# Optimization experiments

Hardware: AMD Instinct MI355X
Metric: run time of the kernel (lower is better)

## Reference

```python
import jax, jax.numpy as jnp
import numpy as np

D_MODEL = 1024
N_HEADS = 16
HEAD_DIM = 64
T = 4096
ROT = HEAD_DIM // 2          # 32 channels get rotary
PAIR = ROT // 2              # 16 cos/sin frequencies
EPS = 1e-6
SCALE = 0.12                 # constant attention scale (not 1/sqrt(d))
ROPE_BASE = 10000.0
VOCAB = 50257


def setup_inputs() -> dict:
    key = jax.random.key(0)
    k_x, k_qkv, k_o, k_tok = jax.random.split(key, 4)
    bound = 0.5 / np.sqrt(D_MODEL)
    x = jax.random.normal(k_x, (1, T, D_MODEL), dtype=jnp.float32)
    w_qkv = jax.random.uniform(k_qkv, (3 * D_MODEL, D_MODEL), jnp.float32, -bound, bound)
    # module uses zero_init for w_o; use small random so output is non-trivial
    w_o = jax.random.uniform(k_o, (D_MODEL, D_MODEL), jnp.float32, -bound, bound)
    q_norm_w = jnp.ones((HEAD_DIM,), jnp.float32)
    k_norm_w = jnp.ones((HEAD_DIM,), jnp.float32)
    tokens = jax.random.randint(k_tok, (1, T), 0, VOCAB, dtype=jnp.int64)
    pos = jnp.arange(T, dtype=jnp.int64)
    # RotaryCache: inv_freq over pair dims, cos/sin of t * inv_freq
    inv_freq = 1.0 / (ROPE_BASE ** (jnp.arange(PAIR, dtype=jnp.float32) / PAIR))
    freqs = jnp.arange(T, dtype=jnp.float32)[:, None] * inv_freq[None, :]  # [T, PAIR]
    return {
        "x": x, "tokens": tokens, "pos": pos,
        "w_qkv": w_qkv, "w_o": w_o,
        "q_norm_w": q_norm_w, "k_norm_w": k_norm_w,
        "cos": jnp.cos(freqs), "sin": jnp.sin(freqs),
        "window_tokens": 1024, "block_size": 128,
    }


def _rmsnorm(x, w):
    var = jnp.mean(x * x, axis=-1, keepdims=True)
    return x * jax.lax.rsqrt(var + EPS) * w


def reference(x, tokens, pos, w_qkv, w_o, q_norm_w, k_norm_w, cos, sin,
              window_tokens, block_size):
    B, Tq, C = x.shape
    H, Dh = N_HEADS, HEAD_DIM
    qkv = x @ w_qkv.T                                  # [B, T, 3C]
    q, k, v = jnp.split(qkv, 3, axis=-1)

    def to_bhtd(t):
        return t.reshape(B, Tq, H, Dh).transpose(0, 2, 1, 3)
    q, k, v = to_bhtd(q), to_bhtd(k), to_bhtd(v)

    q = _rmsnorm(q, q_norm_w)
    k = _rmsnorm(k, k_norm_w)

    # half-truncated RoPE: rotate first ROT channels pairwise (even/odd)
    c = cos[pos][None, None]                           # [1,1,T,PAIR]
    s = sin[pos][None, None]

    def rope_rotate(t):
        t1, t2 = t[..., :ROT], t[..., ROT:]
        even, odd = t1[..., 0::2], t1[..., 1::2]
        r_even = even * c - odd * s
        r_odd = even * s + odd * c
        t1r = jnp.stack([r_even, r_odd], axis=-1).reshape(t1.shape)
        return jnp.concatenate([t1r, t2], axis=-1)

    q = rope_rotate(q)
    k = rope_rotate(k)

    v = v * 0.5                                        # no value-embed branch

    scores = jnp.einsum('bhtd,bhsd->bhts', q, k) * SCALE
    idx = jnp.arange(Tq)
    diff = idx[:, None] - idx[None, :]
    allowed = (diff >= 0) & (diff < window_tokens)     # sliding causal window
    scores = jnp.where(allowed, scores, -jnp.inf)
    p = jax.nn.softmax(scores, axis=-1)
    out = jnp.einsum('bhts,bhsd->bhtd', p, v)
    out = out.transpose(0, 2, 1, 3).reshape(B, Tq, C)
    return out @ w_o.T
```

## Files before the change

### kernel.cpp

```cpp
#include <hip/hip_runtime.h>


typedef __bf16 bf16x8 __attribute__((ext_vector_type(8)));
typedef __bf16 bf16x2 __attribute__((ext_vector_type(2)));
typedef float f32x4 __attribute__((ext_vector_type(4)));
typedef unsigned short u16x8 __attribute__((ext_vector_type(8)));
typedef unsigned short u16x4 __attribute__((ext_vector_type(4)));

#define MFMA16(a, b, c) __builtin_amdgcn_mfma_f32_16x16x32_bf16((a), (b), (c), 0, 0, 0)

__device__ __forceinline__ unsigned short f2bf(float f) {
    unsigned int u = __float_as_uint(f);
    u += 0x7fffu + ((u >> 16) & 1u);
    return (unsigned short)(u >> 16);
}
__device__ __forceinline__ float bf2f(unsigned short h) {
    return __uint_as_float(((unsigned int)h) << 16);
}
__device__ __forceinline__ unsigned int pk2bf(float a, float b) {
#if __has_builtin(__builtin_amdgcn_cvt_pk_bf16_f32)
    bf16x2 v = __builtin_amdgcn_cvt_pk_bf16_f32(a, b);
    return __builtin_bit_cast(unsigned int, v);
#else
    return (unsigned int)f2bf(a) | ((unsigned int)f2bf(b) << 16);
#endif
}

__device__ __forceinline__ void gl_lds16(const void* g, void* l) {
    typedef __attribute__((address_space(1))) unsigned int GU;
    typedef __attribute__((address_space(3))) unsigned int LU;
    __builtin_amdgcn_global_load_lds((GU*)(unsigned long long)g,
                                     (LU*)(unsigned int)(unsigned long long)l,
                                     16, 0, 0);
}

__global__ void cvt3_kernel(const float* __restrict__ x,
                            const float* __restrict__ wqkv,
                            const float* __restrict__ wo,
                            unsigned short* __restrict__ xb,
                            unsigned short* __restrict__ wqkvb,
                            unsigned short* __restrict__ wob) {
    int i = blockIdx.x * 256 + threadIdx.x;
    const float* src;
    unsigned short* dst;
    int off;
    if (i < 1048576) { src = x; dst = xb; off = i; }
    else if (i < 1835008) { src = wqkv; dst = wqkvb; off = i - 1048576; }
    else { src = wo; dst = wob; off = i - 1835008; }
    float4 f = ((const float4*)src)[off];
    u16x4 o;
    o[0] = f2bf(f.x); o[1] = f2bf(f.y); o[2] = f2bf(f.z); o[3] = f2bf(f.w);
    ((u16x4*)dst)[off] = o;
}

#define TBS 72
__global__ __launch_bounds__(256) void gemm_qkv(
    const unsigned short* __restrict__ A,
    const unsigned short* __restrict__ Bt,
    const float* __restrict__ cosb, const float* __restrict__ sinb,
    const float* __restrict__ qw, const float* __restrict__ kw,
    unsigned short* __restrict__ Qb,
    unsigned short* __restrict__ Kb,
    unsigned short* __restrict__ Vt)
{
    __shared__ unsigned short As[2][128 * 32];
    __shared__ unsigned short Bs[2][128 * 32];
    __shared__ unsigned short tb[4][16 * TBS];
    const int tid = threadIdx.x;
    const int wave = tid >> 6, lane = tid & 63;
    const int quad = lane >> 4, l16 = lane & 15;
    const int m0 = blockIdx.x * 128, n0 = blockIdx.y * 128;
    const int wm = (wave >> 1) * 64;

    f32x4 acc[4][4];
#pragma unroll
    for (int i = 0; i < 4; ++i)
#pragma unroll
        for (int j = 0; j < 4; ++j) acc[i][j] = (f32x4){0.f, 0.f, 0.f, 0.f};

    auto stageAB = [&](int buf, int k0) {
#pragma unroll
        for (int i = 0; i < 2; ++i) {
            const int c = wave * 2 + i;
            const int e = (c * 64 + lane) * 8;
            const int r = e >> 5, col = e & 31;
            gl_lds16(A + (size_t)(m0 + r) * 1024 + (k0 + col), &As[buf][c * 512]);
            gl_lds16(Bt + (size_t)(n0 + r) * 1024 + (k0 + col), &Bs[buf][c * 512]);
        }
    };

    stageAB(0, 0);
    __syncthreads();
    int buf = 0;
    for (int k0 = 0; k0 < 1024; k0 += 32) {
        if (k0 + 32 < 1024) stageAB(buf ^ 1, k0 + 32);
        bf16x8 af[4], bfr[4];
#pragma unroll
        for (int mt = 0; mt < 4; ++mt)
            af[mt] = *(const bf16x8*)&As[buf][(wm + mt * 16 + l16) * 32 + quad * 8];
#pragma unroll
        for (int nt = 0; nt < 4; ++nt)
            bfr[nt] = *(const bf16x8*)&Bs[buf][((wave & 1) * 64 + nt * 16 + l16) * 32 + quad * 8];
#pragma unroll
        for (int mt = 0; mt < 4; ++mt)
#pragma unroll
            for (int nt = 0; nt < 4; ++nt)
                acc[mt][nt] = MFMA16(af[mt], bfr[nt], acc[mt][nt]);
        __syncthreads();
        buf ^= 1;
    }

    const int region = blockIdx.y >> 3;
    const int h = ((blockIdx.y & 7) << 1) + (wave & 1);
    unsigned short* tbw = tb[wave];

    if (region < 2) {
        const float* wgt = region ? kw : qw;
        unsigned short* dst = region ? Kb : Qb;
        float w[4];
#pragma unroll
        for (int nt = 0; nt < 4; ++nt) w[nt] = wgt[nt * 16 + l16];
#pragma unroll
        for (int mt = 0; mt < 4; ++mt) {
#pragma unroll
            for (int r = 0; r < 4; ++r) {
                const int row = m0 + wm + mt * 16 + quad * 4 + r;
                float ss = 0.f;
#pragma unroll
                for (int nt = 0; nt < 4; ++nt)
                    ss += acc[mt][nt][r] * acc[mt][nt][r];
                ss += __shfl_xor(ss, 1); ss += __shfl_xor(ss, 2);
                ss += __shfl_xor(ss, 4); ss += __shfl_xor(ss, 8);
                const float rn = rsqrtf(ss * (1.f / 64.f) + 1e-6f);
                float val[4];
#pragma unroll
                for (int nt = 0; nt < 4; ++nt)
                    val[nt] = acc[mt][nt][r] * rn * w[nt];
#pragma unroll
                for (int nt = 0; nt < 2; ++nt) {
                    const float prt = __shfl_xor(val[nt], 1);
                    const int p = nt * 8 + (l16 >> 1);
                    const float c = cosb[row * 16 + p];
                    const float s = sinb[row * 16 + p];
                    val[nt] = (l16 & 1) ? (prt * s + val[nt] * c)
                                        : (val[nt] * c - prt * s);
                }
#pragma unroll
                for (int nt = 0; nt < 4; ++nt)
                    tbw[(quad * 4 + r) * TBS + nt * 16 + l16] = f2bf(val[nt]);
            }
            const int t = lane >> 2, dcol = (lane & 3) * 16;
            u16x8 v0 = *(const u16x8*)&tbw[t * TBS + dcol];
            u16x8 v1 = *(const u16x8*)&tbw[t * TBS + dcol + 8];
            const size_t ob = ((size_t)h * 4096 + (m0 + wm + mt * 16 + t)) * 64 + dcol;
            *(u16x8*)&dst[ob] = v0;
            *(u16x8*)&dst[ob + 8] = v1;
        }
    } else {
#pragma unroll
        for (int mt = 0; mt < 4; ++mt) {
#pragma unroll
            for (int nt = 0; nt < 4; ++nt)
#pragma unroll
                for (int r = 0; r < 4; ++r)
                    tbw[(nt * 16 + l16) * 16 + quad * 4 + r] =
                        f2bf(acc[mt][nt][r] * 0.5f);
            u16x8 v0 = *(const u16x8*)&tbw[lane * 16];
            u16x8 v1 = *(const u16x8*)&tbw[lane * 16 + 8];
            const size_t vo = ((size_t)h * 64 + lane) * 4096 + m0 + wm + mt * 16;
            *(u16x8*)&Vt[vo] = v0;
            *(u16x8*)&Vt[vo + 8] = v1;
        }
    }
}

#define PSTR 72

template <int MODE>
__device__ __forceinline__ void attn_compute(
    int s0, int tq, int quad, int l16,
    const unsigned short* Ks0, const unsigned short* Ks1,
    const unsigned short* Vs0, const unsigned short* Vs1,
    unsigned short* Pw,
    const bf16x8 qf0, const bf16x8 qf1, f32x4 (&o)[4], float& lsum)
{
    const float c = 0.17312340490667046f;
#pragma unroll
    for (int i = 0; i < 4; ++i) {
        const bf16x8 kf0 = *(const bf16x8*)&Ks0[(i * 16 + l16) * 32 + quad * 8];
        const bf16x8 kf1 = *(const bf16x8*)&Ks1[(i * 16 + l16) * 32 + quad * 8];
        f32x4 z = (f32x4){0.f, 0.f, 0.f, 0.f};
        z = MFMA16(kf0, qf0, z);
        z = MFMA16(kf1, qf1, z);
        float p[4];
#pragma unroll
        for (int r = 0; r < 4; ++r) {
            float e = exp2f(z[r] * c);
            if (MODE == 1) {
                const int s = s0 + i * 16 + quad * 4 + r;
                e = ((tq - s) < 1024) ? e : 0.f;
            }
            if (MODE == 2) {
                const int s = s0 + i * 16 + quad * 4 + r;
                e = (s <= tq) ? e : 0.f;
            }
            p[r] = e;
            lsum += e;
        }
        uint2 pk;
        pk.x = pk2bf(p[0], p[1]);
        pk.y = pk2bf(p[2], p[3]);
        *(uint2*)&Pw[l16 * PSTR + i * 16 + quad * 4] = pk;
    }
    const bf16x8 pf0 = *(const bf16x8*)&Pw[l16 * PSTR + quad * 8];
    const bf16x8 pf1 = *(const bf16x8*)&Pw[l16 * PSTR + 32 + quad * 8];
#pragma unroll
    for (int dt = 0; dt < 4; ++dt) {
        const bf16x8 vf0 = *(const bf16x8*)&Vs0[(dt * 16 + l16) * 32 + quad * 8];
        const bf16x8 vf1 = *(const bf16x8*)&Vs1[(dt * 16 + l16) * 32 + quad * 8];
        o[dt] = MFMA16(pf0, vf0, o[dt]);
        o[dt] = MFMA16(pf1, vf1, o[dt]);
    }
}

__global__ __launch_bounds__(256) void attn_kernel(
    const unsigned short* __restrict__ Qb,
    const unsigned short* __restrict__ Kb,
    const unsigned short* __restrict__ Vt,
    unsigned short* __restrict__ att)
{
    __shared__ unsigned short Ks0[2][64 * 32];
    __shared__ unsigned short Ks1[2][64 * 32];
    __shared__ unsigned short Vs0[2][64 * 32];
    __shared__ unsigned short Vs1[2][64 * 32];
    __shared__ unsigned short P[4][16 * PSTR];

    const int bid = blockIdx.x;
    const int h = ((bid & 7) << 1) | ((bid >> 3) & 1);
    const int t0 = (bid >> 4) * 64;

    const int tid = threadIdx.x;
    const int wave = tid >> 6, lane = tid & 63;
    const int quad = lane >> 4, l16 = lane & 15;
    const int qt0 = t0 + wave * 16;
    const int tq = qt0 + l16;
    const int krow = tid >> 2, kcol = (tid & 3) * 8;

    const unsigned short* Qh = Qb + (size_t)h * 4096 * 64;
    const unsigned short* Kh = Kb + (size_t)h * 4096 * 64;
    const unsigned short* Vh = Vt + (size_t)h * 64 * 4096;

    const bf16x8 qf0 = *(const bf16x8*)&Qh[(qt0 + l16) * 64 + quad * 8];
    const bf16x8 qf1 = *(const bf16x8*)&Qh[(qt0 + l16) * 64 + 32 + quad * 8];

    f32x4 o[4];
#pragma unroll
    for (int dt = 0; dt < 4; ++dt) o[dt] = (f32x4){0.f, 0.f, 0.f, 0.f};
    float lsum = 0.f;
    unsigned short* Pw = P[wave];

    auto stage = [&](int buf, int s0) {
        const unsigned short* kb = Kh + (size_t)(s0 + krow) * 64 + kcol;
        const unsigned short* vb = Vh + (size_t)krow * 4096 + s0 + kcol;
        gl_lds16(kb,      &Ks0[buf][wave * 512]);
        gl_lds16(kb + 32, &Ks1[buf][wave * 512]);
        gl_lds16(vb,      &Vs0[buf][wave * 512]);
        gl_lds16(vb + 32, &Vs1[buf][wave * 512]);
    };

    const int sbase = (t0 >= 1024) ? (t0 - 1024) : 0;
    stage(0, sbase);
    __syncthreads();
    int buf = 0;
    for (int s0 = sbase; s0 <= t0; s0 += 64) {
        if (s0 + 64 <= t0) stage(buf ^ 1, s0 + 64);
        if (s0 == sbase && t0 >= 1024)
            attn_compute<1>(s0, tq, quad, l16, Ks0[buf], Ks1[buf], Vs0[buf],
                            Vs1[buf], Pw, qf0, qf1, o, lsum);
        else if (s0 == t0)
            attn_compute<2>(s0, tq, quad, l16, Ks0[buf], Ks1[buf], Vs0[buf],
                            Vs1[buf], Pw, qf0, qf1, o, lsum);
        else
            attn_compute<0>(s0, tq, quad, l16, Ks0[buf], Ks1[buf], Vs0[buf],
                            Vs1[buf], Pw, qf0, qf1, o, lsum);
        __syncthreads();
        buf ^= 1;
    }

    lsum += __shfl_xor(lsum, 16);
    lsum += __shfl_xor(lsum, 32);
    float lr[4];
#pragma unroll
    for (int r = 0; r < 4; ++r) lr[r] = 1.f / __shfl(lsum, quad * 4 + r);
#pragma unroll
    for (int dt = 0; dt < 4; ++dt)
#pragma unroll
        for (int r = 0; r < 4; ++r)
            att[(size_t)(qt0 + quad * 4 + r) * 1024 + h * 64 + dt * 16 + l16] =
                f2bf(o[dt][r] * lr[r]);
}

template <int BM, bool F32OUT>
__global__ __launch_bounds__(256) void gemm_bt(
    const unsigned short* __restrict__ A,
    const unsigned short* __restrict__ Bt,
    void* __restrict__ Cp, int N, int K) {
    __shared__ unsigned short As[2][BM * 32];
    __shared__ unsigned short Bs[2][128 * 32];
    constexpr int MT = BM / 32;
    const int tid = threadIdx.x;
    const int wave = tid >> 6, lane = tid & 63;
    const int quad = lane >> 4, l16 = lane & 15;
    const int m0 = blockIdx.x * BM, n0 = blockIdx.y * 128;
    const int wm = (wave >> 1) * (BM / 2), wn = (wave & 1) * 64;

    f32x4 acc[MT][4];
#pragma unroll
    for (int i = 0; i < MT; ++i)
#pragma unroll
        for (int j = 0; j < 4; ++j) acc[i][j] = (f32x4){0.f, 0.f, 0.f, 0.f};

    auto stageAB = [&](int buf, int k0) {
#pragma unroll
        for (int i = 0; i < BM / 64; ++i) {
            const int c = wave * (BM / 64) + i;
            const int e = (c * 64 + lane) * 8;
            const int r = e >> 5, col = e & 31;
            gl_lds16(A + (size_t)(m0 + r) * K + (k0 + col), &As[buf][c * 512]);
        }
#pragma unroll
        for (int i = 0; i < 2; ++i) {
            const int c = wave * 2 + i;
            const int e = (c * 64 + lane) * 8;
            const int r = e >> 5, col = e & 31;
            gl_lds16(Bt + (size_t)(n0 + r) * K + (k0 + col), &Bs[buf][c * 512]);
        }
    };

    stageAB(0, 0);
    __syncthreads();
    int buf = 0;
    for (int k0 = 0; k0 < K; k0 += 32) {
        if (k0 + 32 < K) stageAB(buf ^ 1, k0 + 32);
        bf16x8 af[MT], bfr[4];
#pragma unroll
        for (int mt = 0; mt < MT; ++mt)
            af[mt] = *(const bf16x8*)&As[buf][(wm + mt * 16 + l16) * 32 + quad * 8];
#pragma unroll
        for (int nt = 0; nt < 4; ++nt)
            bfr[nt] = *(const bf16x8*)&Bs[buf][(wn + nt * 16 + l16) * 32 + quad * 8];
#pragma unroll
        for (int mt = 0; mt < MT; ++mt)
#pragma unroll
            for (int nt = 0; nt < 4; ++nt)
                acc[mt][nt] = MFMA16(af[mt], bfr[nt], acc[mt][nt]);
        __syncthreads();
        buf ^= 1;
    }
#pragma unroll
    for (int mt = 0; mt < MT; ++mt)
#pragma unroll
        for (int nt = 0; nt < 4; ++nt)
#pragma unroll
            for (int r = 0; r < 4; ++r) {
                const int row = m0 + wm + mt * 16 + quad * 4 + r;
                const int col = n0 + wn + nt * 16 + l16;
                const float v = acc[mt][nt][r];
                if (F32OUT)
                    ((float*)Cp)[(size_t)row * N + col] = v;
                else
                    ((unsigned short*)Cp)[(size_t)row * N + col] = f2bf(v);
            }
}

extern "C" void kernel_launch(void* const* d_in, const int* in_sizes, int n_in,
                              void* d_out, int out_size, void* d_ws, size_t ws_size,
                              hipStream_t stream) {
    const float* x    = (const float*)d_in[0];
    const float* wqkv = (const float*)d_in[3];
    const float* wo   = (const float*)d_in[4];
    const float* qw   = (const float*)d_in[5];
    const float* kw   = (const float*)d_in[6];
    const float* cosb = (const float*)d_in[7];
    const float* sinb = (const float*)d_in[8];

    char* ws = (char*)d_ws;
    if (ws_size < (size_t)48 * 1024 * 1024) return;
    unsigned short* xb    = (unsigned short*)(ws + ((size_t)0 << 20));
    unsigned short* wqkvb = (unsigned short*)(ws + ((size_t)8 << 20));
    unsigned short* wob   = (unsigned short*)(ws + ((size_t)14 << 20));
    unsigned short* Qb    = (unsigned short*)(ws + ((size_t)16 << 20));
    unsigned short* Kb    = (unsigned short*)(ws + ((size_t)24 << 20));
    unsigned short* Vt    = (unsigned short*)(ws + ((size_t)32 << 20));
    unsigned short* attb  = (unsigned short*)(ws + ((size_t)40 << 20));

    cvt3_kernel<<<8192, 256, 0, stream>>>(x, wqkv, wo, xb, wqkvb, wob);

    gemm_qkv<<<dim3(32, 24), 256, 0, stream>>>(xb, wqkvb, cosb, sinb, qw, kw,
                                               Qb, Kb, Vt);

    attn_kernel<<<1024, 256, 0, stream>>>(Qb, Kb, Vt, attb);

    gemm_bt<64, true><<<dim3(64, 8), 256, 0, stream>>>(attb, wob, (float*)d_out, 1024, 1024);
}
```

Baseline: 192.5 us.

## Single-buffer attention tiles, fold softmax scale into Q, reverse block order

```diff
diff --git a/kernel.cpp b/kernel.cpp
--- a/kernel.cpp
+++ b/kernel.cpp
@@ -23,6 +23,13 @@
     return __builtin_bit_cast(unsigned int, v);
 #else
     return (unsigned int)f2bf(a) | ((unsigned int)f2bf(b) << 16);
+#endif
+}
+__device__ __forceinline__ float fexp2(float x) {
+#if __has_builtin(__builtin_amdgcn_exp2f)
+    return __builtin_amdgcn_exp2f(x);
+#else
+    return exp2f(x);
 #endif
 }
 
@@ -117,9 +124,10 @@
     if (region < 2) {
         const float* wgt = region ? kw : qw;
         unsigned short* dst = region ? Kb : Qb;
+        const float post = region ? 1.f : 0.17312340490667046f;
         float w[4];
 #pragma unroll
-        for (int nt = 0; nt < 4; ++nt) w[nt] = wgt[nt * 16 + l16];
+        for (int nt = 0; nt < 4; ++nt) w[nt] = wgt[nt * 16 + l16] * post;
 #pragma unroll
         for (int mt = 0; mt < 4; ++mt) {
 #pragma unroll
@@ -177,14 +185,22 @@
 #define PSTR 72
 
 template <int MODE>
-__device__ __forceinline__ void attn_compute(
-    int s0, int tq, int quad, int l16,
-    const unsigned short* Ks0, const unsigned short* Ks1,
-    const unsigned short* Vs0, const unsigned short* Vs1,
-    unsigned short* Pw,
+__device__ __forceinline__ void attn_step(
+    int s0, int tq, int wave, int quad, int l16, int krow, int kcol,
+    const unsigned short* __restrict__ Kh, const unsigned short* __restrict__ Vh,
+    unsigned short* Ks0, unsigned short* Ks1,
+    unsigned short* Vs0, unsigned short* Vs1, unsigned short* Pw,
     const bf16x8 qf0, const bf16x8 qf1, f32x4 (&o)[4], float& lsum)
 {
-    const float c = 0.17312340490667046f;
+    __syncthreads();
+    const unsigned short* kb = Kh + (size_t)(s0 + krow) * 64 + kcol;
+    const unsigned short* vb = Vh + (size_t)krow * 4096 + s0 + kcol;
+    gl_lds16(kb,      &Ks0[wave * 512]);
+    gl_lds16(kb + 32, &Ks1[wave * 512]);
+    gl_lds16(vb,      &Vs0[wave * 512]);
+    gl_lds16(vb + 32, &Vs1[wave * 512]);
+    __syncthreads();
+
 #pragma unroll
     for (int i = 0; i < 4; ++i) {
         const bf16x8 kf0 = *(const bf16x8*)&Ks0[(i * 16 + l16) * 32 + quad * 8];
@@ -195,7 +211,7 @@
         float p[4];
 #pragma unroll
         for (int r = 0; r < 4; ++r) {
-            float e = exp2f(z[r] * c);
+            float e = fexp2(z[r]);
             if (MODE == 1) {
                 const int s = s0 + i * 16 + quad * 4 + r;
                 e = ((tq - s) < 1024) ? e : 0.f;
@@ -229,15 +245,15 @@
     const unsigned short* __restrict__ Vt,
     unsigned short* __restrict__ att)
 {
-    __shared__ unsigned short Ks0[2][64 * 32];
-    __shared__ unsigned short Ks1[2][64 * 32];
-    __shared__ unsigned short Vs0[2][64 * 32];
-    __shared__ unsigned short Vs1[2][64 * 32];
+    __shared__ unsigned short Ks0[64 * 32];
+    __shared__ unsigned short Ks1[64 * 32];
+    __shared__ unsigned short Vs0[64 * 32];
+    __shared__ unsigned short Vs1[64 * 32];
     __shared__ unsigned short P[4][16 * PSTR];
 
     const int bid = blockIdx.x;
     const int h = ((bid & 7) << 1) | ((bid >> 3) & 1);
-    const int t0 = (bid >> 4) * 64;
+    const int t0 = (63 - (bid >> 4)) * 64;
 
     const int tid = threadIdx.x;
     const int wave = tid >> 6, lane = tid & 63;
@@ -259,33 +275,17 @@
     float lsum = 0.f;
     unsigned short* Pw = P[wave];
 
-    auto stage = [&](int buf, int s0) {
-        const unsigned short* kb = Kh + (size_t)(s0 + krow) * 64 + kcol;
-        const unsigned short* vb = Vh + (size_t)krow * 4096 + s0 + kcol;
-        gl_lds16(kb,      &Ks0[buf][wave * 512]);
-        gl_lds16(kb + 32, &Ks1[buf][wave * 512]);
-        gl_lds16(vb,      &Vs0[buf][wave * 512]);
-        gl_lds16(vb + 32, &Vs1[buf][wave * 512]);
-    };
-
-    const int sbase = (t0 >= 1024) ? (t0 - 1024) : 0;
-    stage(0, sbase);
-    __syncthreads();
-    int buf = 0;
-    for (int s0 = sbase; s0 <= t0; s0 += 64) {
-        if (s0 + 64 <= t0) stage(buf ^ 1, s0 + 64);
-        if (s0 == sbase && t0 >= 1024)
-            attn_compute<1>(s0, tq, quad, l16, Ks0[buf], Ks1[buf], Vs0[buf],
-                            Vs1[buf], Pw, qf0, qf1, o, lsum);
-        else if (s0 == t0)
-            attn_compute<2>(s0, tq, quad, l16, Ks0[buf], Ks1[buf], Vs0[buf],
-                            Vs1[buf], Pw, qf0, qf1, o, lsum);
-        else
-            attn_compute<0>(s0, tq, quad, l16, Ks0[buf], Ks1[buf], Vs0[buf],
-                            Vs1[buf], Pw, qf0, qf1, o, lsum);
-        __syncthreads();
-        buf ^= 1;
-    }
+    int s0 = (t0 >= 1024) ? (t0 - 1024) : 0;
+    if (t0 >= 1024) {
+        attn_step<1>(s0, tq, wave, quad, l16, krow, kcol, Kh, Vh,
+                     Ks0, Ks1, Vs0, Vs1, Pw, qf0, qf1, o, lsum);
+        s0 += 64;
+    }
+    for (; s0 < t0; s0 += 64)
+        attn_step<0>(s0, tq, wave, quad, l16, krow, kcol, Kh, Vh,
+                     Ks0, Ks1, Vs0, Vs1, Pw, qf0, qf1, o, lsum);
+    attn_step<2>(t0, tq, wave, quad, l16, krow, kcol, Kh, Vh,
+                 Ks0, Ks1, Vs0, Vs1, Pw, qf0, qf1, o, lsum);
 
     lsum += __shfl_xor(lsum, 16);
     lsum += __shfl_xor(lsum, 32);
```

Result: faster. 185.6 us (-3.6%).
